# Kernel tuning notes

Measured on AMD Instinct MI355X. Metric: run time of the kernel, lower is better.

## Reference

```python
import math
import jax, jax.numpy as jnp
import numpy as np

RES = [16, 32, 64, 128, 256, 512, 1024, 2048]  # base=16, finest=2048, 8 levels, growth=2
FD = 2            # feature_dim per grid level
LPE_N = 128
NF = 4            # lpe_n_freq
D0 = 8            # lpe_d0
LPE_OUT = D0 + 4 * NF  # 24
HID = 64
T = 4             # num_textures
EPS = 1e-6


def _gather_bilerp(grid, u, v, scale, imax, stride):
    """Bilinear gather from a flattened 2D grid. Returns (feat[B,C], lu[B,1], lv[B,1])."""
    fu = u * scale
    fv = v * scale
    i0 = jnp.clip(jnp.floor(fu).astype(jnp.int32), 0, imax)
    j0 = jnp.clip(jnp.floor(fv).astype(jnp.int32), 0, imax)
    lu = (fu - i0.astype(fu.dtype))[:, None]
    lv = (fv - j0.astype(fv.dtype))[:, None]
    idx00 = i0 + j0 * stride
    f00 = grid[idx00]
    f10 = grid[idx00 + 1]
    f01 = grid[idx00 + stride]
    f11 = grid[idx00 + 1 + stride]
    f0 = f00 * (1.0 - lu) + f10 * lu
    f1 = f01 * (1.0 - lu) + f11 * lu
    return f0 * (1.0 - lv) + f1 * lv, lu, lv


def setup_inputs() -> dict:
    key = jax.random.key(0)
    ks = jax.random.split(key, 24)
    B = 1048576
    inp = {"coords": jax.random.uniform(ks[0], (B, 2), jnp.float32)}
    for i, r in enumerate(RES):
        inp[f"grid{i}"] = jax.random.uniform(ks[1 + i], (r * r, FD), jnp.float32, -1e-4, 1e-4)
    inp["lpe_grid"] = jax.random.uniform(ks[9], ((LPE_N + 1) ** 2, LPE_OUT), jnp.float32, -1e-4, 1e-4)
    in_dim = FD + LPE_OUT  # 26
    inp["w0"] = jax.random.normal(ks[10], (in_dim, HID), jnp.float32) / math.sqrt(in_dim)
    inp["b0"] = jnp.zeros((HID,), jnp.float32)
    inp["w1"] = jax.random.normal(ks[11], (HID, HID), jnp.float32) / math.sqrt(HID)
    inp["b1"] = jnp.zeros((HID,), jnp.float32)
    inp["w2"] = jax.random.normal(ks[12], (HID, T), jnp.float32) / math.sqrt(HID)
    inp["b2"] = jnp.zeros((T,), jnp.float32)
    return inp


def _forward(coords, grids, lpe_grid, w0, b0, w1, b1, w2, b2):
    c = jnp.clip(coords, 0.0, 1.0 - EPS)
    u = c[:, 0]
    v = c[:, 1]
    # Multi-resolution feature grids, residual-fused (sum over levels)
    enc = jnp.zeros((coords.shape[0], FD), jnp.float32)
    for r, g in zip(RES, grids):
        f, _, _ = _gather_bilerp(g, u, v, float(r - 1), r - 2, r)
        enc = enc + f
    # Local positional encoding on (N+1)^2 grid
    coeff, lu, lv = _gather_bilerp(lpe_grid, u, v, float(LPE_N), LPE_N - 1, LPE_N + 1)
    freqs = (2.0 ** jnp.arange(NF, dtype=jnp.float32)) * (2.0 * math.pi)  # [NF]
    uu = lu * freqs[None, :]
    vv = lv * freqs[None, :]
    pe = jnp.concatenate([jnp.cos(uu), jnp.sin(uu), jnp.cos(vv), jnp.sin(vv)], axis=1)  # [B,4*NF]
    base = coeff[:, :D0]
    gate = coeff[:, D0:D0 + 4 * NF]
    lpe_out = jnp.concatenate([base, gate * pe], axis=1)  # [B,LPE_OUT]
    feat = jnp.concatenate([enc, lpe_out], axis=1)  # [B,26]
    h = jax.nn.relu(feat @ w0 + b0)
    h = jax.nn.relu(h @ w1 + b1)
    return jax.nn.sigmoid(h @ w2 + b2)  # [B,T]


def reference(coords, grid0, grid1, grid2, grid3, grid4, grid5, grid6, grid7,
              lpe_grid, w0, b0, w1, b1, w2, b2):
    grids = (grid0, grid1, grid2, grid3, grid4, grid5, grid6, grid7)
    return _forward(coords, grids, lpe_grid, w0, b0, w1, b1, w2, b2)
```

## Files before the change

### kernel.cpp

```cpp
#include <hip/hip_runtime.h>
#include <hip/hip_bf16.h>
#include <math.h>

typedef short bf16x8 __attribute__((ext_vector_type(8)));
typedef float f32x16 __attribute__((ext_vector_type(16)));
typedef float f32x4 __attribute__((ext_vector_type(4)));
typedef float f32x2 __attribute__((ext_vector_type(2)));
typedef unsigned u32x4 __attribute__((ext_vector_type(4)));

#define NF 4
#define D0 8
#define LPE_OUT 24
#define NBUCKET 512
#define NROWS   512

#define PART_OFF   17408ULL
#define TOT_OFF    1065984ULL
#define LPE_OFF    1068544ULL
#define SCOORD_OFF 1867776ULL
#define PERM_OFF   10256384ULL
#define G6B_OFF    14450688ULL
#define G7B_OFF    18644992ULL
#define WS_NEED    35422208ULL

__device__ __forceinline__ unsigned f2bf(float x) {
    unsigned u = __float_as_uint(x);
    u = u + 0x7fffu + ((u >> 16) & 1u);
    return u >> 16;
}
__device__ __forceinline__ unsigned pkbf(float a, float b) {
    __hip_bfloat16 ha = __float2bfloat16(a);
    __hip_bfloat16 hb = __float2bfloat16(b);
    unsigned short ua, ub;
    __builtin_memcpy(&ua, &ha, 2);
    __builtin_memcpy(&ub, &hb, 2);
    return (unsigned)ua | ((unsigned)ub << 16);
}
__device__ __forceinline__ float bflo(unsigned u) { return __uint_as_float(u << 16); }
__device__ __forceinline__ float bfhi(unsigned u) { return __uint_as_float(u & 0xffff0000u); }
__device__ __forceinline__ f32x2 bf2(unsigned u) { f32x2 r = { bflo(u), bfhi(u) }; return r; }
__device__ __forceinline__ bf16x8 mkfrag(unsigned w0, unsigned w1, unsigned w2, unsigned w3) {
    u32x4 u = { w0, w1, w2, w3 };
    return __builtin_bit_cast(bf16x8, u);
}

__device__ void prep_body(const float* __restrict__ w0, const float* __restrict__ b0,
                          const float* __restrict__ w1, const float* __restrict__ b1,
                          const float* __restrict__ w2, float* __restrict__ ws, int t)
{
    unsigned short* a0 = (unsigned short*)ws;
    unsigned short* a1 = a0 + 2048;
    unsigned short* a2 = a1 + 4096;
    float* b0c = (float*)(a2 + 2048);
    float* b1c = b0c + 64;

    for (int e = t; e < 2048; e += 256) {
        int tile = e >> 9, lane = (e >> 3) & 63, j = e & 7;
        int m = tile >> 1, ks = tile & 1;
        int row = m * 32 + (lane & 31);
        int k = ks * 16 + (lane >> 5) * 8 + j;
        float v = (k < 26) ? w0[k * 64 + row] : 0.f;
        a0[e] = (unsigned short)f2bf(v);
    }
    for (int e = t; e < 4096; e += 256) {
        int tile = e >> 9, lane = (e >> 3) & 63, j = e & 7;
        int m = tile >> 2, ks = tile & 3;
        int row = m * 32 + (lane & 31);
        int k = ks * 16 + (lane >> 5) * 8 + j;
        a1[e] = (unsigned short)f2bf(w1[k * 64 + row]);
    }
    for (int e = t; e < 2048; e += 256) {
        int ks = e >> 9, lane = (e >> 3) & 63, j = e & 7;
        int row = lane & 31;
        int k = ks * 16 + (lane >> 5) * 8 + j;
        float v = (row < 4) ? w2[k * 4 + row] : 0.f;
        a2[e] = (unsigned short)f2bf(v);
    }
    if (t < 64) {
        int m = t >> 5, q5 = (t >> 4) & 1, r = t & 15;
        int row = (r & 3) + 8 * (r >> 2) + 4 * q5;
        b0c[(m * 2 + q5) * 16 + r] = b0[m * 32 + row];
        b1c[(m * 2 + q5) * 16 + r] = b1[m * 32 + row];
    }
}

__global__ void prep_kernel(const float* __restrict__ w0, const float* __restrict__ b0,
                            const float* __restrict__ w1, const float* __restrict__ b1,
                            const float* __restrict__ w2, float* __restrict__ ws)
{
    prep_body(w0, b0, w1, b1, w2, ws, threadIdx.x);
}

__device__ __forceinline__ int bucket_of(float cx, float cy) {
    float u = fminf(fmaxf(cx, 0.f), 1.f - 1e-6f);
    float v = fminf(fmaxf(cy, 0.f), 1.f - 1e-6f);
    return (int)(v * 32.f) * 16 + (int)(u * 16.f);
}

__global__ __launch_bounds__(256)
void fused_pre(const float2* __restrict__ g6, const float2* __restrict__ g7,
               const float4* __restrict__ lpe4, const float2* __restrict__ coords,
               unsigned* __restrict__ part, unsigned* __restrict__ totals,
               const float* __restrict__ w0, const float* __restrict__ b0,
               const float* __restrict__ w1, const float* __restrict__ b1,
               const float* __restrict__ w2, float* __restrict__ ws, char* __restrict__ wsb)
{
    int b = blockIdx.x, t = threadIdx.x;
    if (b < 16384) {
        int cell = b * 256 + t;
        float2 f = g7[cell];
        ((unsigned*)(wsb + G7B_OFF))[cell] = pkbf(f.x, f.y);
        return;
    }
    if (b < 20480) {
        int cell = (b - 16384) * 256 + t;
        float2 f = g6[cell];
        ((unsigned*)(wsb + G6B_OFF))[cell] = pkbf(f.x, f.y);
        return;
    }
    if (b < 20676) {
        int i = (b - 20480) * 256 + t;
        if (i < 49923) {
            float4 a = lpe4[i * 2], c = lpe4[i * 2 + 1];
            u32x4 o = { pkbf(a.x, a.y), pkbf(a.z, a.w), pkbf(c.x, c.y), pkbf(c.z, c.w) };
            ((u32x4*)(wsb + LPE_OFF))[i] = o;
        }
        return;
    }
    if (b < 21188) {
        int hb = b - 20676;
        __shared__ unsigned h[NBUCKET];
        h[t] = 0; h[t + 256] = 0;
        __syncthreads();
        for (int k = 0; k < 8; ++k) {
            float2 c = coords[hb * 2048 + k * 256 + t];
            atomicAdd(&h[bucket_of(c.x, c.y)], 1u);
        }
        __syncthreads();
        unsigned v0 = h[t], v1 = h[t + 256];
        part[hb * NBUCKET + t] = v0;
        part[hb * NBUCKET + 256 + t] = v1;
        if (v0) atomicAdd(&totals[t], v0);
        if (v1) atomicAdd(&totals[t + 256], v1);
        return;
    }
    prep_body(w0, b0, w1, b1, w2, ws, t);
}

__global__ __launch_bounds__(256)
void sort_offsets(unsigned* __restrict__ part, const unsigned* __restrict__ totals)
{
    int bucket = blockIdx.x, t = threadIdx.x;
    __shared__ unsigned red[256];
    unsigned s0 = (t < bucket) ? totals[t] : 0u;
    if (t + 256 < bucket) s0 += totals[t + 256];
    red[t] = s0;
    __syncthreads();
    for (int off = 128; off > 0; off >>= 1) {
        if (t < off) red[t] += red[t + off];
        __syncthreads();
    }
    unsigned start = red[0];
    __syncthreads();

    unsigned l0 = part[(2 * t) * NBUCKET + bucket];
    unsigned l1 = part[(2 * t + 1) * NBUCKET + bucket];
    unsigned s = l0 + l1;
    __shared__ unsigned sc[256];
    sc[t] = s;
    __syncthreads();
    for (int off = 1; off < 256; off <<= 1) {
        unsigned v = (t >= off) ? sc[t - off] : 0u;
        __syncthreads();
        sc[t] += v;
        __syncthreads();
    }
    unsigned base = start + sc[t] - s;
    part[(2 * t) * NBUCKET + bucket] = base;
    part[(2 * t + 1) * NBUCKET + bucket] = base + l0;
}

__global__ __launch_bounds__(256)
void sort_scatter(const float2* __restrict__ coords, const unsigned* __restrict__ offs,
                  float2* __restrict__ scoord, unsigned* __restrict__ perm)
{
    __shared__ unsigned cnt[NBUCKET];
    __shared__ unsigned base[NBUCKET];
    int t = threadIdx.x, hb = blockIdx.x;
    cnt[t] = 0; cnt[t + 256] = 0;
    base[t] = offs[hb * NBUCKET + t];
    base[t + 256] = offs[hb * NBUCKET + 256 + t];
    __syncthreads();
    for (int k = 0; k < 8; ++k) {
        int i = hb * 2048 + k * 256 + t;
        float2 c = coords[i];
        int bb = bucket_of(c.x, c.y);
        unsigned r = atomicAdd(&cnt[bb], 1u);
        unsigned slot = base[bb] + r;
        scoord[slot] = c;
        perm[slot] = (unsigned)i;
    }
}

__device__ __forceinline__ void mlp_pair(const unsigned (&B0)[2][2][4],
                                         const float* __restrict__ ws,
                                         const float* __restrict__ b2,
                                         int lane, int q5, f32x16 (&acc2)[2])
{
    const bf16x8* A0 = (const bf16x8*)ws;
    const bf16x8* A1 = (const bf16x8*)((const char*)ws + 4096);
    const bf16x8* A2 = (const bf16x8*)((const char*)ws + 12288);
    const float4* b0c = (const float4*)((const char*)ws + 16384);
    const float4* b1c = (const float4*)((const char*)ws + 16640);

    unsigned B1[4][2][4];
#pragma unroll
    for (int m = 0; m < 2; ++m) {
        f32x16 acc[2];
#pragma unroll
        for (int cc = 0; cc < 4; ++cc) {
            float4 bq = b0c[(m * 2 + q5) * 4 + cc];
#pragma unroll
            for (int n = 0; n < 2; ++n) {
                acc[n][4 * cc + 0] = bq.x;
                acc[n][4 * cc + 1] = bq.y;
                acc[n][4 * cc + 2] = bq.z;
                acc[n][4 * cc + 3] = bq.w;
            }
        }
#pragma unroll
        for (int ks = 0; ks < 2; ++ks) {
            bf16x8 af = A0[(m * 2 + ks) * 64 + lane];
#pragma unroll
            for (int n = 0; n < 2; ++n)
                acc[n] = __builtin_amdgcn_mfma_f32_32x32x16_bf16(
                    af, mkfrag(B0[ks][n][0], B0[ks][n][1], B0[ks][n][2], B0[ks][n][3]),
                    acc[n], 0, 0, 0);
        }
#pragma unroll
        for (int t = 0; t < 2; ++t) {
#pragma unroll
            for (int n = 0; n < 2; ++n)
#pragma unroll
                for (int c = 0; c < 2; ++c) {
                    int r0 = 2 * c + 8 * t;
                    int r1 = 2 * c + 8 * t + 4;
                    unsigned P0 = pkbf(fmaxf(acc[n][r0], 0.f), fmaxf(acc[n][r0 + 1], 0.f));
                    unsigned P1 = pkbf(fmaxf(acc[n][r1], 0.f), fmaxf(acc[n][r1 + 1], 0.f));
                    auto r = __builtin_amdgcn_permlane32_swap(P1, P0, false, false);
                    B1[2 * m + t][n][c] = r[1];
                    B1[2 * m + t][n][2 + c] = r[0];
                }
        }
    }

    unsigned B2[4][2][4];
#pragma unroll
    for (int m = 0; m < 2; ++m) {
        f32x16 acc[2];
#pragma unroll
        for (int cc = 0; cc < 4; ++cc) {
            float4 bq = b1c[(m * 2 + q5) * 4 + cc];
#pragma unroll
            for (int n = 0; n < 2; ++n) {
                acc[n][4 * cc + 0] = bq.x;
                acc[n][4 * cc + 1] = bq.y;
                acc[n][4 * cc + 2] = bq.z;
                acc[n][4 * cc + 3] = bq.w;
            }
        }
#pragma unroll
        for (int ks = 0; ks < 4; ++ks) {
            bf16x8 af = A1[(m * 4 + ks) * 64 + lane];
#pragma unroll
            for (int n = 0; n < 2; ++n)
                acc[n] = __builtin_amdgcn_mfma_f32_32x32x16_bf16(
                    af, mkfrag(B1[ks][n][0], B1[ks][n][1], B1[ks][n][2], B1[ks][n][3]),
                    acc[n], 0, 0, 0);
        }
#pragma unroll
        for (int t = 0; t < 2; ++t) {
#pragma unroll
            for (int n = 0; n < 2; ++n)
#pragma unroll
                for (int c = 0; c < 2; ++c) {
                    int r0 = 2 * c + 8 * t;
                    int r1 = 2 * c + 8 * t + 4;
                    unsigned P0 = pkbf(fmaxf(acc[n][r0], 0.f), fmaxf(acc[n][r0 + 1], 0.f));
                    unsigned P1 = pkbf(fmaxf(acc[n][r1], 0.f), fmaxf(acc[n][r1 + 1], 0.f));
                    auto r = __builtin_amdgcn_permlane32_swap(P1, P0, false, false);
                    B2[2 * m + t][n][c] = r[1];
                    B2[2 * m + t][n][2 + c] = r[0];
                }
        }
    }

#pragma unroll
    for (int n = 0; n < 2; ++n)
#pragma unroll
        for (int r = 0; r < 16; ++r) acc2[n][r] = (r < 4) ? b2[r] : 0.f;
#pragma unroll
    for (int ks = 0; ks < 4; ++ks) {
        bf16x8 af = A2[ks * 64 + lane];
#pragma unroll
        for (int n = 0; n < 2; ++n)
            acc2[n] = __builtin_amdgcn_mfma_f32_32x32x16_bf16(
                af, mkfrag(B2[ks][n][0], B2[ks][n][1], B2[ks][n][2], B2[ks][n][3]),
                acc2[n], 0, 0, 0);
    }
}

__global__ __launch_bounds__(256, 4)
void colornet_sorted(const float2* __restrict__ pts,
                     const unsigned* __restrict__ perm,
                     const f32x2* __restrict__ g0, const f32x2* __restrict__ g1,
                     const f32x2* __restrict__ g2, const f32x2* __restrict__ g3,
                     const f32x2* __restrict__ g4, const f32x2* __restrict__ g5,
                     const float* __restrict__ ws,
                     const float* __restrict__ b2,
                     f32x4* __restrict__ out)
{
    const int lane = threadIdx.x & 63;
    const int wave = threadIdx.x >> 6;
    const int q5 = lane >> 5;
    int bid = blockIdx.x;
    int cpx = gridDim.x >> 3;
    bid = (bid & 7) * cpx + (bid >> 3);
    const int base_pt = bid * 256 + wave * 64;
    const char* wsb = (const char*)ws;

    float2 c = pts[base_pt + lane];
    float uA = fminf(fmaxf(c.x, 0.f), 1.f - 1e-6f);
    float vA = fminf(fmaxf(c.y, 0.f), 1.f - 1e-6f);

#define ADDR(IDX, R) int gx##IDX; float lu##IDX, lv##IDX; \
    { float fu_ = uA * (float)((R) - 1), fv_ = vA * (float)((R) - 1); \
      int i0_ = (int)floorf(fu_), j0_ = (int)floorf(fv_); \
      i0_ = i0_ < 0 ? 0 : (i0_ > (R) - 2 ? (R) - 2 : i0_); \
      j0_ = j0_ < 0 ? 0 : (j0_ > (R) - 2 ? (R) - 2 : j0_); \
      lu##IDX = fu_ - (float)i0_; lv##IDX = fv_ - (float)j0_; \
      gx##IDX = i0_ + j0_ * (R); }
    ADDR(7, 2048) ADDR(6, 1024) ADDR(5, 512) ADDR(4, 256)
    ADDR(3, 128)  ADDR(2, 64)   ADDR(1, 32)  ADDR(0, 16)

    const unsigned* G7 = (const unsigned*)(wsb + G7B_OFF);
    const unsigned* G6 = (const unsigned*)(wsb + G6B_OFF);
    unsigned t7_0 = G7[gx7], t7_1 = G7[gx7 + 1], t7_2 = G7[gx7 + 2048], t7_3 = G7[gx7 + 2049];
    unsigned t6_0 = G6[gx6], t6_1 = G6[gx6 + 1], t6_2 = G6[gx6 + 1024], t6_3 = G6[gx6 + 1025];

#define LOADF(IDX, R, G) \
    f32x2 f##IDX##_0 = (G)[gx##IDX],       f##IDX##_1 = (G)[gx##IDX + 1], \
          f##IDX##_2 = (G)[gx##IDX + (R)], f##IDX##_3 = (G)[gx##IDX + (R) + 1];
    LOADF(5, 512, g5) LOADF(4, 256, g4) LOADF(3, 128, g3)
    LOADF(2, 64,  g2) LOADF(1, 32,  g1) LOADF(0, 16,  g0)

    float lu_pe, lv_pe;
    int lc;
    {
        float fu = uA * 128.f, fv = vA * 128.f;
        int i0 = (int)floorf(fu);
        int j0 = (int)floorf(fv);
        i0 = i0 < 0 ? 0 : (i0 > 127 ? 127 : i0);
        j0 = j0 < 0 ? 0 : (j0 > 127 ? 127 : j0);
        lu_pe = fu - (float)i0;
        lv_pe = fv - (float)j0;
        lc = (i0 + j0 * 129) * 3;
    }
    const u32x4* LP = (const u32x4*)(wsb + LPE_OFF);
    u32x4 L00a = LP[lc],       L00b = LP[lc + 1],   L00c = LP[lc + 2];
    u32x4 L10a = LP[lc + 3],   L10b = LP[lc + 4],   L10c = LP[lc + 5];
    u32x4 L01a = LP[lc + 387], L01b = LP[lc + 388], L01c = LP[lc + 389];
    u32x4 L11a = LP[lc + 390], L11b = LP[lc + 391], L11c = LP[lc + 392];

    float pe[16];
#pragma unroll
    for (int kf = 0; kf < NF; ++kf) {
        float au = lu_pe * (float)(1 << kf);
        float av = lv_pe * (float)(1 << kf);
        float fu_ = __builtin_amdgcn_fractf(au);
        float fv_ = __builtin_amdgcn_fractf(av);
        pe[kf]          = __builtin_amdgcn_cosf(fu_);
        pe[NF + kf]     = __builtin_amdgcn_sinf(fu_);
        pe[2 * NF + kf] = __builtin_amdgcn_cosf(fv_);
        pe[3 * NF + kf] = __builtin_amdgcn_sinf(fv_);
    }

    f32x2 eA = { 0.f, 0.f };
#define WGT(IDX) float omu##IDX = 1.f - lu##IDX, omv##IDX = 1.f - lv##IDX; \
    float w00##IDX = omu##IDX * omv##IDX, w10##IDX = lu##IDX * omv##IDX, \
          w01##IDX = omu##IDX * lv##IDX,  w11##IDX = lu##IDX * lv##IDX;
    { WGT(7)
      eA += bf2(t7_0) * w007 + bf2(t7_1) * w107 + bf2(t7_2) * w017 + bf2(t7_3) * w117; }
    { WGT(6)
      eA += bf2(t6_0) * w006 + bf2(t6_1) * w106 + bf2(t6_2) * w016 + bf2(t6_3) * w116; }
#define SUMF(IDX) { WGT(IDX) \
      eA += f##IDX##_0 * w00##IDX + f##IDX##_1 * w10##IDX + f##IDX##_2 * w01##IDX + f##IDX##_3 * w11##IDX; }
    SUMF(5) SUMF(4) SUMF(3) SUMF(2) SUMF(1) SUMF(0)

    f32x2 cf[12];
    {
        float omu = 1.f - lu_pe, omv = 1.f - lv_pe;
        float q00 = omu * omv, q10 = lu_pe * omv, q01 = omu * lv_pe, q11 = lu_pe * lv_pe;
#define LPW2(W, A, B, C, Dd) \
        cf[W] = bf2(A) * q00 + bf2(B) * q10 + bf2(C) * q01 + bf2(Dd) * q11;
        LPW2(0,  L00a[0], L10a[0], L01a[0], L11a[0])
        LPW2(1,  L00a[1], L10a[1], L01a[1], L11a[1])
        LPW2(2,  L00a[2], L10a[2], L01a[2], L11a[2])
        LPW2(3,  L00a[3], L10a[3], L01a[3], L11a[3])
        LPW2(4,  L00b[0], L10b[0], L01b[0], L11b[0])
        LPW2(5,  L00b[1], L10b[1], L01b[1], L11b[1])
        LPW2(6,  L00b[2], L10b[2], L01b[2], L11b[2])
        LPW2(7,  L00b[3], L10b[3], L01b[3], L11b[3])
        LPW2(8,  L00c[0], L10c[0], L01c[0], L11c[0])
        LPW2(9,  L00c[1], L10c[1], L01c[1], L11c[1])
        LPW2(10, L00c[2], L10c[2], L01c[2], L11c[2])
        LPW2(11, L00c[3], L10c[3], L01c[3], L11c[3])
#undef LPW2
    }

    unsigned fdA[16];
    fdA[0] = pkbf(eA[0], eA[1]);
#pragma unroll
    for (int i = 0; i < 4; ++i) fdA[1 + i] = pkbf(cf[i][0], cf[i][1]);
#pragma unroll
    for (int i = 0; i < 8; ++i) {
        f32x2 g = { pe[2 * i], pe[2 * i + 1] };
        f32x2 m = cf[4 + i] * g;
        fdA[5 + i] = pkbf(m[0], m[1]);
    }
    fdA[13] = 0u; fdA[14] = 0u; fdA[15] = 0u;

    unsigned B0a[2][2][4];
#pragma unroll
    for (int ks = 0; ks < 2; ++ks)
#pragma unroll
        for (int j2 = 0; j2 < 4; ++j2) {
            unsigned a = fdA[8 * ks + j2];
            unsigned b = fdA[8 * ks + 4 + j2];
            auto r = __builtin_amdgcn_permlane32_swap(b, a, false, false);
            B0a[ks][1][j2] = r[0];
            B0a[ks][0][j2] = r[1];
        }

    f32x16 acc2[2];
    mlp_pair(B0a, ws, b2, lane, q5, acc2);

    if (lane < 32) {
#pragma unroll
        for (int n = 0; n < 2; ++n) {
            f32x4 o;
            o[0] = 1.f / (1.f + __expf(-acc2[n][0]));
            o[1] = 1.f / (1.f + __expf(-acc2[n][1]));
            o[2] = 1.f / (1.f + __expf(-acc2[n][2]));
            o[3] = 1.f / (1.f + __expf(-acc2[n][3]));
            int oi = (int)perm[base_pt + 32 * n + lane];
            __builtin_nontemporal_store(o, out + oi);
        }
    }
}

template<int R>
__device__ __forceinline__ void gather_level(const float* __restrict__ g,
                                             float u, float v,
                                             float& e0, float& e1) {
    const float scale = (float)(R - 1);
    float fu = u * scale, fv = v * scale;
    int i0 = (int)floorf(fu);
    int j0 = (int)floorf(fv);
    i0 = i0 < 0 ? 0 : (i0 > R - 2 ? R - 2 : i0);
    j0 = j0 < 0 ? 0 : (j0 > R - 2 ? R - 2 : j0);
    float lu = fu - (float)i0;
    float lv = fv - (float)j0;
    const float2* gg = (const float2*)g;
    int base = i0 + j0 * R;
    float2 f00 = gg[base];
    float2 f10 = gg[base + 1];
    float2 f01 = gg[base + R];
    float2 f11 = gg[base + R + 1];
    float omu = 1.f - lu, omv = 1.f - lv;
    float w00 = omu * omv, w10 = lu * omv, w01 = omu * lv, w11 = lu * lv;
    e0 += f00.x * w00 + f10.x * w10 + f01.x * w01 + f11.x * w11;
    e1 += f00.y * w00 + f10.y * w10 + f01.y * w01 + f11.y * w11;
}

__global__ __launch_bounds__(256, 4)
void colornet_fp32(const float* __restrict__ coords,
                   const float* __restrict__ g0, const float* __restrict__ g1,
                   const float* __restrict__ g2, const float* __restrict__ g3,
                   const float* __restrict__ g4, const float* __restrict__ g5,
                   const float* __restrict__ g6, const float* __restrict__ g7,
                   const float* __restrict__ lpe,
                   const float* __restrict__ ws,
                   const float* __restrict__ b2,
                   f32x4* __restrict__ out)
{
    const int lane = threadIdx.x & 63;
    const int wave = threadIdx.x >> 6;
    const int q5 = lane >> 5;
    const int base_pt = blockIdx.x * 256 + wave * 64;
    const int point = base_pt + lane;

    const float* cp = coords + 2 * point;
    float cx = __builtin_nontemporal_load(cp);
    float cy = __builtin_nontemporal_load(cp + 1);
    float uA = fminf(fmaxf(cx, 0.f), 1.f - 1e-6f);
    float vA = fminf(fmaxf(cy, 0.f), 1.f - 1e-6f);

    float e0 = 0.f, e1 = 0.f;
    gather_level<16>(g0, uA, vA, e0, e1);
    gather_level<32>(g1, uA, vA, e0, e1);
    gather_level<64>(g2, uA, vA, e0, e1);
    gather_level<128>(g3, uA, vA, e0, e1);
    gather_level<256>(g4, uA, vA, e0, e1);
    gather_level<512>(g5, uA, vA, e0, e1);
    gather_level<1024>(g6, uA, vA, e0, e1);
    gather_level<2048>(g7, uA, vA, e0, e1);

    float coeff[LPE_OUT];
    float lu_pe, lv_pe;
    {
        float fu = uA * 128.f, fv = vA * 128.f;
        int i0 = (int)floorf(fu);
        int j0 = (int)floorf(fv);
        i0 = i0 < 0 ? 0 : (i0 > 127 ? 127 : i0);
        j0 = j0 < 0 ? 0 : (j0 > 127 ? 127 : j0);
        lu_pe = fu - (float)i0;
        lv_pe = fv - (float)j0;
        int base = (i0 + j0 * 129) * LPE_OUT;
        const float4* p00 = (const float4*)(lpe + base);
        const float4* p10 = (const float4*)(lpe + base + LPE_OUT);
        const float4* p01 = (const float4*)(lpe + base + 129 * LPE_OUT);
        const float4* p11 = (const float4*)(lpe + base + 130 * LPE_OUT);
        float omu = 1.f - lu_pe, omv = 1.f - lv_pe;
        float w00 = omu * omv, w10 = lu_pe * omv, w01 = omu * lv_pe, w11 = lu_pe * lv_pe;
#pragma unroll
        for (int q = 0; q < 6; ++q) {
            float4 a = p00[q], bq = p10[q], cq = p01[q], dq = p11[q];
            coeff[4 * q + 0] = a.x * w00 + bq.x * w10 + cq.x * w01 + dq.x * w11;
            coeff[4 * q + 1] = a.y * w00 + bq.y * w10 + cq.y * w01 + dq.y * w11;
            coeff[4 * q + 2] = a.z * w00 + bq.z * w10 + cq.z * w01 + dq.z * w11;
            coeff[4 * q + 3] = a.w * w00 + bq.w * w10 + cq.w * w01 + dq.w * w11;
        }
    }

    float pe[16];
#pragma unroll
    for (int kf = 0; kf < NF; ++kf) {
        const float fr = 6.28318530717958647692f * (float)(1 << kf);
        float au = lu_pe * fr;
        float av = lv_pe * fr;
        pe[kf]          = __cosf(au);
        pe[NF + kf]     = __sinf(au);
        pe[2 * NF + kf] = __cosf(av);
        pe[3 * NF + kf] = __sinf(av);
    }

    float feat[32];
    feat[0] = e0; feat[1] = e1;
#pragma unroll
    for (int q = 0; q < D0; ++q) feat[2 + q] = coeff[q];
#pragma unroll
    for (int q = 0; q < 4 * NF; ++q) feat[2 + D0 + q] = coeff[D0 + q] * pe[q];
#pragma unroll
    for (int q = 26; q < 32; ++q) feat[q] = 0.f;

    unsigned fd[16];
#pragma unroll
    for (int i = 0; i < 16; ++i) fd[i] = pkbf(feat[2 * i], feat[2 * i + 1]);

    unsigned B0[2][2][4];
#pragma unroll
    for (int ks = 0; ks < 2; ++ks)
#pragma unroll
        for (int j2 = 0; j2 < 4; ++j2) {
            unsigned a = fd[8 * ks + j2];
            unsigned b = fd[8 * ks + 4 + j2];
            auto r = __builtin_amdgcn_permlane32_swap(b, a, false, false);
            B0[ks][1][j2] = r[0];
            B0[ks][0][j2] = r[1];
        }

    f32x16 acc2[2];
    mlp_pair(B0, ws, b2, lane, q5, acc2);
    if (lane < 32) {
#pragma unroll
        for (int n = 0; n < 2; ++n) {
            f32x4 o;
            o[0] = 1.f / (1.f + __expf(-acc2[n][0]));
            o[1] = 1.f / (1.f + __expf(-acc2[n][1]));
            o[2] = 1.f / (1.f + __expf(-acc2[n][2]));
            o[3] = 1.f / (1.f + __expf(-acc2[n][3]));
            __builtin_nontemporal_store(o, out + (base_pt + 32 * n + lane));
        }
    }
}

extern "C" void kernel_launch(void* const* d_in, const int* in_sizes, int n_in,
                              void* d_out, int out_size, void* d_ws, size_t ws_size,
                              hipStream_t stream) {
    const float* coords = (const float*)d_in[0];
    const float* g0 = (const float*)d_in[1];
    const float* g1 = (const float*)d_in[2];
    const float* g2 = (const float*)d_in[3];
    const float* g3 = (const float*)d_in[4];
    const float* g4 = (const float*)d_in[5];
    const float* g5 = (const float*)d_in[6];
    const float* g6 = (const float*)d_in[7];
    const float* g7 = (const float*)d_in[8];
    const float* lpe = (const float*)d_in[9];
    const float* w0 = (const float*)d_in[10];
    const float* b0 = (const float*)d_in[11];
    const float* w1 = (const float*)d_in[12];
    const float* b1 = (const float*)d_in[13];
    const float* w2 = (const float*)d_in[14];
    const float* b2 = (const float*)d_in[15];
    f32x4* out = (f32x4*)d_out;

    int B = in_sizes[0] / 2;
    char* wsb = (char*)d_ws;

    if (ws_size >= WS_NEED && B == 1048576) {
        unsigned* part   = (unsigned*)(wsb + PART_OFF);
        unsigned* totals = (unsigned*)(wsb + TOT_OFF);
        float2*   scoord = (float2*)(wsb + SCOORD_OFF);
        unsigned* perm   = (unsigned*)(wsb + PERM_OFF);
        const float2* c2 = (const float2*)coords;

        (void)hipMemsetAsync(totals, 0, NBUCKET * sizeof(unsigned), stream);
        fused_pre<<<21189, 256, 0, stream>>>((const float2*)g6, (const float2*)g7,
                                             (const float4*)lpe, c2, part, totals,
                                             w0, b0, w1, b1, w2, (float*)d_ws, wsb);
        sort_offsets<<<NBUCKET, 256, 0, stream>>>(part, totals);
        sort_scatter<<<NROWS, 256, 0, stream>>>(c2, part, scoord, perm);

        colornet_sorted<<<4096, 256, 0, stream>>>(scoord, perm,
                                                  (const f32x2*)g0, (const f32x2*)g1,
                                                  (const f32x2*)g2, (const f32x2*)g3,
                                                  (const f32x2*)g4, (const f32x2*)g5,
                                                  (const float*)d_ws, b2, out);
    } else {
        prep_kernel<<<1, 256, 0, stream>>>(w0, b0, w1, b1, w2, (float*)d_ws);
        colornet_fp32<<<B / 256, 256, 0, stream>>>(coords, g0, g1, g2, g3, g4, g5, g6, g7,
                                                   lpe, (const float*)d_ws, b2, out);
    }
}
```

Before: 126.3 us.

## Replace per-block offset kernel with global atomic cursors in bucket scatter

Drops the sort_offsets kernel and the per-block partial histogram array. Each scatter block now computes the bucket prefix sum from the global totals itself and reserves its slot range per bucket with an atomicAdd on a global cursor array. This saves a kernel launch and the partial-count traffic, at the cost of a redundant 512-entry scan in every block and nondeterministic ordering within each bucket.

```diff
diff --git a/kernel.cpp b/kernel.cpp
--- a/kernel.cpp
+++ b/kernel.cpp
@@ -14,8 +14,7 @@
 #define NBUCKET 512
 #define NROWS   512
 
-#define PART_OFF   17408ULL
-#define TOT_OFF    1065984ULL
+#define TOTC_OFF   17408ULL
 #define LPE_OFF    1068544ULL
 #define SCOORD_OFF 1867776ULL
 #define PERM_OFF   10256384ULL
@@ -100,7 +99,7 @@
 __global__ __launch_bounds__(256)
 void fused_pre(const float2* __restrict__ g6, const float2* __restrict__ g7,
                const float4* __restrict__ lpe4, const float2* __restrict__ coords,
-               unsigned* __restrict__ part, unsigned* __restrict__ totals,
+               unsigned* __restrict__ totals,
                const float* __restrict__ w0, const float* __restrict__ b0,
                const float* __restrict__ w1, const float* __restrict__ b1,
                const float* __restrict__ w2, float* __restrict__ ws, char* __restrict__ wsb)
@@ -138,8 +137,6 @@
         }
         __syncthreads();
         unsigned v0 = h[t], v1 = h[t + 256];
-        part[hb * NBUCKET + t] = v0;
-        part[hb * NBUCKET + 256 + t] = v1;
         if (v0) atomicAdd(&totals[t], v0);
         if (v1) atomicAdd(&totals[t + 256], v1);
         return;
@@ -148,57 +145,49 @@
 }
 
 __global__ __launch_bounds__(256)
-void sort_offsets(unsigned* __restrict__ part, const unsigned* __restrict__ totals)
-{
-    int bucket = blockIdx.x, t = threadIdx.x;
-    __shared__ unsigned red[256];
-    unsigned s0 = (t < bucket) ? totals[t] : 0u;
-    if (t + 256 < bucket) s0 += totals[t + 256];
-    red[t] = s0;
-    __syncthreads();
-    for (int off = 128; off > 0; off >>= 1) {
-        if (t < off) red[t] += red[t + off];
-        __syncthreads();
-    }
-    unsigned start = red[0];
-    __syncthreads();
-
-    unsigned l0 = part[(2 * t) * NBUCKET + bucket];
-    unsigned l1 = part[(2 * t + 1) * NBUCKET + bucket];
-    unsigned s = l0 + l1;
-    __shared__ unsigned sc[256];
-    sc[t] = s;
-    __syncthreads();
-    for (int off = 1; off < 256; off <<= 1) {
-        unsigned v = (t >= off) ? sc[t - off] : 0u;
-        __syncthreads();
-        sc[t] += v;
-        __syncthreads();
-    }
-    unsigned base = start + sc[t] - s;
-    part[(2 * t) * NBUCKET + bucket] = base;
-    part[(2 * t + 1) * NBUCKET + bucket] = base + l0;
-}
-
-__global__ __launch_bounds__(256)
-void sort_scatter(const float2* __restrict__ coords, const unsigned* __restrict__ offs,
+void sort_scatter(const float2* __restrict__ coords,
+                  const unsigned* __restrict__ totals, unsigned* __restrict__ cursor,
                   float2* __restrict__ scoord, unsigned* __restrict__ perm)
 {
+    __shared__ unsigned ps[NBUCKET];
     __shared__ unsigned cnt[NBUCKET];
-    __shared__ unsigned base[NBUCKET];
+    __shared__ unsigned rnk[NBUCKET];
+    __shared__ unsigned basev[NBUCKET];
     int t = threadIdx.x, hb = blockIdx.x;
+
+    unsigned o0 = totals[t], o1 = totals[t + 256];
+    ps[t] = o0; ps[t + 256] = o1;
     cnt[t] = 0; cnt[t + 256] = 0;
-    base[t] = offs[hb * NBUCKET + t];
-    base[t + 256] = offs[hb * NBUCKET + 256 + t];
+    rnk[t] = 0; rnk[t + 256] = 0;
     __syncthreads();
+    for (int off = 1; off < 512; off <<= 1) {
+        unsigned v0 = (t >= off) ? ps[t - off] : 0u;
+        unsigned v1 = (t + 256 >= off) ? ps[t + 256 - off] : 0u;
+        __syncthreads();
+        ps[t] += v0; ps[t + 256] += v1;
+        __syncthreads();
+    }
+
+    float2 cpt[8]; int bkt[8];
+#pragma unroll
     for (int k = 0; k < 8; ++k) {
-        int i = hb * 2048 + k * 256 + t;
-        float2 c = coords[i];
-        int bb = bucket_of(c.x, c.y);
-        unsigned r = atomicAdd(&cnt[bb], 1u);
-        unsigned slot = base[bb] + r;
-        scoord[slot] = c;
-        perm[slot] = (unsigned)i;
+        cpt[k] = coords[hb * 2048 + k * 256 + t];
+        bkt[k] = bucket_of(cpt[k].x, cpt[k].y);
+        atomicAdd(&cnt[bkt[k]], 1u);
+    }
+    __syncthreads();
+
+    unsigned c0 = cnt[t], c1 = cnt[t + 256];
+    if (c0) basev[t]       = (ps[t] - o0)       + atomicAdd(&cursor[t], c0);
+    if (c1) basev[t + 256] = (ps[t + 256] - o1) + atomicAdd(&cursor[t + 256], c1);
+    __syncthreads();
+
+#pragma unroll
+    for (int k = 0; k < 8; ++k) {
+        unsigned r = atomicAdd(&rnk[bkt[k]], 1u);
+        unsigned slot = basev[bkt[k]] + r;
+        scoord[slot] = cpt[k];
+        perm[slot] = (unsigned)(hb * 2048 + k * 256 + t);
     }
 }
 
@@ -620,18 +609,17 @@
     char* wsb = (char*)d_ws;
 
     if (ws_size >= WS_NEED && B == 1048576) {
-        unsigned* part   = (unsigned*)(wsb + PART_OFF);
-        unsigned* totals = (unsigned*)(wsb + TOT_OFF);
+        unsigned* totals = (unsigned*)(wsb + TOTC_OFF);
+        unsigned* cursor = totals + NBUCKET;
         float2*   scoord = (float2*)(wsb + SCOORD_OFF);
         unsigned* perm   = (unsigned*)(wsb + PERM_OFF);
         const float2* c2 = (const float2*)coords;
 
-        (void)hipMemsetAsync(totals, 0, NBUCKET * sizeof(unsigned), stream);
+        (void)hipMemsetAsync(totals, 0, 2 * NBUCKET * sizeof(unsigned), stream);
         fused_pre<<<21189, 256, 0, stream>>>((const float2*)g6, (const float2*)g7,
-                                             (const float4*)lpe, c2, part, totals,
+                                             (const float4*)lpe, c2, totals,
                                              w0, b0, w1, b1, w2, (float*)d_ws, wsb);
-        sort_offsets<<<NBUCKET, 256, 0, stream>>>(part, totals);
-        sort_scatter<<<NROWS, 256, 0, stream>>>(c2, part, scoord, perm);
+        sort_scatter<<<NROWS, 256, 0, stream>>>(c2, totals, cursor, scoord, perm);
 
         colornet_sorted<<<4096, 256, 0, stream>>>(scoord, perm,
                                                   (const f32x2*)g0, (const f32x2*)g1,
```

Result: no change. 125.1 us (-0.9%).
